# Performance work log

Hardware: AMD Instinct MI355X
Metric: run time of the kernel (lower is better)

## Reference

```python
import jax, jax.numpy as jnp
import numpy as np
import math

B, S, H, N = 64, 512, 768, 16
C_COMP, C_REL = 5, 3
P = N * (N - 1)
LN_EPS = 1e-5

# ordered pair indices (i, j), i != j, row-major like the torch double loop
_PAIR_I, _PAIR_J = np.nonzero(~np.eye(N, dtype=bool))
_PAIR_I = jnp.asarray(_PAIR_I)
_PAIR_J = jnp.asarray(_PAIR_J)


def setup_inputs() -> dict:
    key = jax.random.key(0)
    ks = jax.random.split(key, 20)
    sc = 0.02
    p = lambda k, shape: (jax.random.normal(k, shape, jnp.float32) * sc)
    return {
        "last_hidden_state": jax.random.normal(ks[0], (B, S, H), jnp.float32),
        "span_starts": jax.random.randint(ks[1], (B, N), 0, 480).astype(jnp.int32),
        "span_lengths": jax.random.randint(ks[2], (B, N), 0, 31).astype(jnp.int32),
        "components": jax.random.randint(ks[3], (B, N), 0, C_COMP).astype(jnp.int32),
        "relations": jax.random.randint(ks[4], (B, P), 0, C_REL).astype(jnp.int32),
        # comp_classifier: Linear(H,512) -> Tanh -> Linear(512,C_COMP)
        "comp_w1": p(ks[5], (H, 512)), "comp_b1": jnp.zeros((512,), jnp.float32),
        "comp_w2": p(ks[6], (512, C_COMP)), "comp_b2": jnp.zeros((C_COMP,), jnp.float32),
        # Attention(H, H), no bias
        "wq": p(ks[7], (H, H)), "wk": p(ks[8], (H, H)), "wv": p(ks[9], (H, H)),
        # LayerNorm(H)
        "ln_g": jnp.ones((H,), jnp.float32), "ln_b": jnp.zeros((H,), jnp.float32),
        # rel_classifier: Linear(2H,512) -> Tanh -> Linear(512,C_REL)
        "rel_w1": p(ks[10], (2 * H, 512)), "rel_b1": jnp.zeros((512,), jnp.float32),
        "rel_w2": p(ks[11], (512, C_REL)), "rel_b2": jnp.zeros((C_REL,), jnp.float32),
    }


def _ce_mean(logits, gold):
    # logits [M, C], gold [M] -> scalar mean cross entropy
    logp = jax.nn.log_softmax(logits, axis=-1)
    return -jnp.mean(jnp.take_along_axis(logp, gold[:, None].astype(jnp.int32), axis=-1))


def reference(last_hidden_state, span_starts, span_lengths, components, relations,
              comp_w1, comp_b1, comp_w2, comp_b2,
              wq, wk, wv, ln_g, ln_b,
              rel_w1, rel_b1, rel_w2, rel_b2):
    # --- per-span mean pooling (inclusive end = start + length), masked+vectorized ---
    pos = jnp.arange(S)
    ends = span_starts + span_lengths
    mask = ((pos[None, None, :] >= span_starts[:, :, None]) &
            (pos[None, None, :] <= ends[:, :, None])).astype(jnp.float32)  # [B,N,S]
    lens = (span_lengths + 1).astype(jnp.float32)
    pooled = jnp.einsum('bns,bsh->bnh', mask, last_hidden_state) / lens[:, :, None]  # [B,N,H]
    # dropout(p=0.2) is identity in eval mode

    # --- component classifier ---
    comp_logits = jnp.tanh(pooled @ comp_w1 + comp_b1) @ comp_w2 + comp_b2  # [B,N,C_COMP]

    # --- small self-attention over spans ---
    q = pooled @ wq; k = pooled @ wk; v = pooled @ wv
    scores = jax.nn.softmax(jnp.einsum('bnd,bmd->bnm', q, k) / math.sqrt(H), axis=-1)
    attn = jnp.einsum('bnm,bmh->bnh', scores, v)

    # --- residual + layernorm ---
    x = pooled + attn
    mu = jnp.mean(x, axis=-1, keepdims=True)
    var = jnp.mean((x - mu) ** 2, axis=-1, keepdims=True)
    x = (x - mu) * jax.lax.rsqrt(var + LN_EPS) * ln_g + ln_b  # [B,N,H]

    # --- O(N^2) pairwise relation classification (ordered pairs i != j) ---
    pair_feat = jnp.concatenate([x[:, _PAIR_I, :], x[:, _PAIR_J, :]], axis=-1)  # [B,P,2H]
    rel_logits = jnp.tanh(pair_feat @ rel_w1 + rel_b1) @ rel_w2 + rel_b2  # [B,P,C_REL]

    loss_comp = _ce_mean(comp_logits.reshape(-1, C_COMP), components.reshape(-1))
    loss_rel = _ce_mean(rel_logits.reshape(-1, C_REL), relations.reshape(-1))
    return (comp_logits.reshape(-1, C_COMP), rel_logits.reshape(-1, C_REL), loss_comp, loss_rel)
```

## Files before the change

### kernel.cpp

```cpp
#include <hip/hip_runtime.h>

#define BB 64
#define SS 512
#define HH 768
#define PP 240
#define CCOMP 5

typedef unsigned short u16;
typedef __attribute__((ext_vector_type(8))) short bf16x8;
typedef __attribute__((ext_vector_type(4))) float f32x4;

__device__ __forceinline__ u16 f2bf(float f) {
    union { float f; unsigned int i; } v; v.f = f;
    unsigned int x = v.i;
    unsigned int lsb = (x >> 16) & 1u;
    x += 0x7fffu + lsb;
    return (u16)(x >> 16);
}

__device__ __forceinline__ float ftanh(float x) {
    float xc = fminf(fmaxf(x, -15.f), 15.f);
    float e = __expf(2.f * xc);
    return (e - 1.f) / (e + 1.f);
}

__device__ __forceinline__ void gl_lds16(const void* g, void* l) {
    __builtin_amdgcn_global_load_lds(
        (const __attribute__((address_space(1))) unsigned int*)g,
        (__attribute__((address_space(3))) unsigned int*)l, 16, 0, 0);
}

__global__ __launch_bounds__(256) void prep_pool_kernel(
    const float* __restrict__ lhs, const int* __restrict__ starts,
    const int* __restrict__ lens, float* __restrict__ pooled, u16* __restrict__ pooled_bf,
    const float* __restrict__ cw1, const float* __restrict__ wq,
    const float* __restrict__ wk, const float* __restrict__ wv,
    const float* __restrict__ rw1, u16* __restrict__ wcat_t, u16* __restrict__ relw_t) {
    int blk = blockIdx.x;
    int tid = threadIdx.x;
    if (blk < 1024) {
        if (tid >= 192) return;
        int st = starts[blk];
        int ln = lens[blk];
        int b = blk >> 4;
        const float4* base = (const float4*)(lhs + ((size_t)b * SS + st) * HH);
        float4 a = {0.f, 0.f, 0.f, 0.f};
        for (int s = 0; s <= ln; ++s) {
            float4 v = base[s * 192 + tid];
            a.x += v.x; a.y += v.y; a.z += v.z; a.w += v.w;
        }
        float inv = 1.0f / (float)(ln + 1);
        a.x *= inv; a.y *= inv; a.z *= inv; a.w *= inv;
        *(float4*)(pooled + (size_t)blk * HH + tid * 4) = a;
        ushort4 ub = { f2bf(a.x), f2bf(a.y), f2bf(a.z), f2bf(a.w) };
        *(ushort4*)(pooled_bf + (size_t)blk * HH + tid * 4) = ub;
        return;
    }
    blk -= 1024;
    const float* W; int ldw, nt; u16* outp;
    if (blk < 384)        {             W = cw1; ldw = 512; nt = 16; outp = wcat_t; }
    else if (blk < 960)   { blk -= 384; W = wq;  ldw = 768; nt = 24; outp = wcat_t + (size_t)512 * 768; }
    else if (blk < 1536)  { blk -= 960; W = wk;  ldw = 768; nt = 24; outp = wcat_t + (size_t)1280 * 768; }
    else if (blk < 2112)  { blk -= 1536; W = wv; ldw = 768; nt = 24; outp = wcat_t + (size_t)2048 * 768; }
    else if (blk < 2496)  { blk -= 2112; W = rw1; ldw = 512; nt = 16; outp = relw_t; }
    else                  { blk -= 2496; W = rw1 + (size_t)768 * 512; ldw = 512; nt = 16; outp = relw_t + (size_t)512 * 768; }
    int tk = blk / nt, tn = blk % nt;
    int k0 = tk * 32, n0 = tn * 32;
    __shared__ u16 Ls[32][36];
    int tx = tid & 31, ty = tid >> 5;
#pragma unroll
    for (int r = 0; r < 4; ++r) {
        int k = ty + r * 8;
        Ls[tx][k] = f2bf(W[(size_t)(k0 + k) * ldw + n0 + tx]);
    }
    __syncthreads();
#pragma unroll
    for (int r = 0; r < 4; ++r) {
        int n = ty + r * 8;
        outp[(size_t)(n0 + n) * 768 + k0 + tx] = Ls[n][tx];
    }
}

__global__ __launch_bounds__(256) void gemm_pw_kernel(
    const u16* __restrict__ pooled_bf, const u16* __restrict__ wcat_t,
    const float* __restrict__ comp_b1, float* __restrict__ y2) {
    __shared__ u16 As[2][4096];
    __shared__ u16 Bs[2][4096];
    int bid = blockIdx.x;
    int sw = (bid & 7) * 88 + (bid >> 3);
    int ct = sw >> 4;
    int rt = sw & 15;
    int ccol0 = ct * 64, row0 = rt * 64;
    int act = (ccol0 < 512);
    int tid = threadIdx.x;
    int lane = tid & 63, w = tid >> 6;
    int q = lane >> 4, l15 = lane & 15;
    int wm = (w & 1) * 32, wn = (w >> 1) * 32;

    int srow = w * 8 + (lane >> 3);
    int sxs = ((lane & 7) * 16) ^ ((srow & 7) << 4);
    const char* gA0 = (const char*)(pooled_bf + (size_t)(row0 + srow) * 768) + sxs;
    const char* gA1 = gA0 + (size_t)32 * 768 * 2;
    const char* gB0 = (const char*)(wcat_t + (size_t)(ccol0 + srow) * 768) + sxs;
    const char* gB1 = gB0 + (size_t)32 * 768 * 2;
    char* lA = (char*)As + w * 1024;
    char* lB = (char*)Bs + w * 1024;

    f32x4 acc[2][2];
#pragma unroll
    for (int i = 0; i < 2; ++i)
#pragma unroll
        for (int j = 0; j < 2; ++j) acc[i][j] = (f32x4){0.f, 0.f, 0.f, 0.f};

#define STAGE_PW(BUF, KB) do { \
        gl_lds16(gA0 + (KB), lA + (BUF) * 8192); \
        gl_lds16(gA1 + (KB), lA + (BUF) * 8192 + 4096); \
        gl_lds16(gB0 + (KB), lB + (BUF) * 8192); \
        gl_lds16(gB1 + (KB), lB + (BUF) * 8192 + 4096); \
    } while (0)

    STAGE_PW(0, 0);
    asm volatile("s_waitcnt vmcnt(0)" ::: "memory");
    __syncthreads();
    int cur = 0;
    for (int t = 0; t < 12; ++t) {
        if (t < 11) STAGE_PW(cur ^ 1, (t + 1) * 128);
        const char* Ab = (const char*)As + cur * 8192;
        const char* Bb = (const char*)Bs + cur * 8192;
#pragma unroll
        for (int ks = 0; ks < 2; ++ks) {
            int o = ks * 64 + q * 16;
            int Ra0 = wm + l15, Ra1 = wm + 16 + l15;
            int Rb0 = wn + l15, Rb1 = wn + 16 + l15;
            bf16x8 a0 = *(const bf16x8*)(Ab + Ra0 * 128 + (o ^ ((Ra0 & 7) << 4)));
            bf16x8 a1 = *(const bf16x8*)(Ab + Ra1 * 128 + (o ^ ((Ra1 & 7) << 4)));
            bf16x8 b0 = *(const bf16x8*)(Bb + Rb0 * 128 + (o ^ ((Rb0 & 7) << 4)));
            bf16x8 b1 = *(const bf16x8*)(Bb + Rb1 * 128 + (o ^ ((Rb1 & 7) << 4)));
            acc[0][0] = __builtin_amdgcn_mfma_f32_16x16x32_bf16(a0, b0, acc[0][0], 0, 0, 0);
            acc[0][1] = __builtin_amdgcn_mfma_f32_16x16x32_bf16(a0, b1, acc[0][1], 0, 0, 0);
            acc[1][0] = __builtin_amdgcn_mfma_f32_16x16x32_bf16(a1, b0, acc[1][0], 0, 0, 0);
            acc[1][1] = __builtin_amdgcn_mfma_f32_16x16x32_bf16(a1, b1, acc[1][1], 0, 0, 0);
        }
        asm volatile("s_waitcnt vmcnt(0)" ::: "memory");
        __syncthreads();
        cur ^= 1;
    }
#pragma unroll
    for (int tm = 0; tm < 2; ++tm)
#pragma unroll
        for (int tn = 0; tn < 2; ++tn)
#pragma unroll
            for (int reg = 0; reg < 4; ++reg) {
                int rr = row0 + wm + tm * 16 + q * 4 + reg;
                int cc = ccol0 + wn + tn * 16 + l15;
                float v = acc[tm][tn][reg];
                if (act) v = ftanh(v + comp_b1[cc]);
                y2[(size_t)rr * 2816 + cc] = v;
            }
}

__global__ __launch_bounds__(256) void gemm_z_kernel(
    const u16* __restrict__ x_bf, const u16* __restrict__ relw_t, float* __restrict__ Z) {
    __shared__ u16 As[2][4096];
    __shared__ u16 Bs[2][4096];
    int bid = blockIdx.x;
    int sw = (bid & 7) * 32 + (bid >> 3);
    int ct = sw >> 4;
    int rt = sw & 15;
    int ccol0 = ct * 64, row0 = rt * 64;
    int tid = threadIdx.x;
    int lane = tid & 63, w = tid >> 6;
    int q = lane >> 4, l15 = lane & 15;
    int wm = (w & 1) * 32, wn = (w >> 1) * 32;

    int srow = w * 8 + (lane >> 3);
    int sxs = ((lane & 7) * 16) ^ ((srow & 7) << 4);
    const char* gA0 = (const char*)(x_bf + (size_t)(row0 + srow) * 768) + sxs;
    const char* gA1 = gA0 + (size_t)32 * 768 * 2;
    const char* gB0 = (const char*)(relw_t + (size_t)(ccol0 + srow) * 768) + sxs;
    const char* gB1 = gB0 + (size_t)32 * 768 * 2;
    char* lA = (char*)As + w * 1024;
    char* lB = (char*)Bs + w * 1024;

    f32x4 acc[2][2];
#pragma unroll
    for (int i = 0; i < 2; ++i)
#pragma unroll
        for (int j = 0; j < 2; ++j) acc[i][j] = (f32x4){0.f, 0.f, 0.f, 0.f};

    STAGE_PW(0, 0);
    asm volatile("s_waitcnt vmcnt(0)" ::: "memory");
    __syncthreads();
    int cur = 0;
    for (int t = 0; t < 12; ++t) {
        if (t < 11) STAGE_PW(cur ^ 1, (t + 1) * 128);
        const char* Ab = (const char*)As + cur * 8192;
        const char* Bb = (const char*)Bs + cur * 8192;
#pragma unroll
        for (int ks = 0; ks < 2; ++ks) {
            int o = ks * 64 + q * 16;
            int Ra0 = wm + l15, Ra1 = wm + 16 + l15;
            int Rb0 = wn + l15, Rb1 = wn + 16 + l15;
            bf16x8 a0 = *(const bf16x8*)(Ab + Ra0 * 128 + (o ^ ((Ra0 & 7) << 4)));
            bf16x8 a1 = *(const bf16x8*)(Ab + Ra1 * 128 + (o ^ ((Ra1 & 7) << 4)));
            bf16x8 b0 = *(const bf16x8*)(Bb + Rb0 * 128 + (o ^ ((Rb0 & 7) << 4)));
            bf16x8 b1 = *(const bf16x8*)(Bb + Rb1 * 128 + (o ^ ((Rb1 & 7) << 4)));
            acc[0][0] = __builtin_amdgcn_mfma_f32_16x16x32_bf16(a0, b0, acc[0][0], 0, 0, 0);
            acc[0][1] = __builtin_amdgcn_mfma_f32_16x16x32_bf16(a0, b1, acc[0][1], 0, 0, 0);
            acc[1][0] = __builtin_amdgcn_mfma_f32_16x16x32_bf16(a1, b0, acc[1][0], 0, 0, 0);
            acc[1][1] = __builtin_amdgcn_mfma_f32_16x16x32_bf16(a1, b1, acc[1][1], 0, 0, 0);
        }
        asm volatile("s_waitcnt vmcnt(0)" ::: "memory");
        __syncthreads();
        cur ^= 1;
    }
#pragma unroll
    for (int tm = 0; tm < 2; ++tm)
#pragma unroll
        for (int tn = 0; tn < 2; ++tn)
#pragma unroll
            for (int reg = 0; reg < 4; ++reg) {
                int rr = row0 + wm + tm * 16 + q * 4 + reg;
                int cc = ccol0 + wn + tn * 16 + l15;
                Z[(size_t)rr * 1024 + cc] = acc[tm][tn][reg];
            }
}

__global__ __launch_bounds__(256) void attn_ln_kernel(
    const float* __restrict__ y2, const float* __restrict__ pooled,
    const float* __restrict__ ln_g, const float* __restrict__ ln_b,
    u16* __restrict__ x_bf) {
    int w = threadIdx.x >> 6, l = threadIdx.x & 63;
    int gw = blockIdx.x * 4 + w;
    int b = gw >> 4, n = gw & 15;
    const float* qrow = y2 + (size_t)(b * 16 + n) * 2816 + 512;
    float qv[12];
#pragma unroll
    for (int u = 0; u < 12; ++u) qv[u] = qrow[l + 64 * u];

    float s[16];
#pragma unroll
    for (int m = 0; m < 16; ++m) {
        const float* krow = y2 + (size_t)(b * 16 + m) * 2816 + 1280;
        float p = 0.f;
#pragma unroll
        for (int u = 0; u < 12; ++u) p += qv[u] * krow[l + 64 * u];
#pragma unroll
        for (int off = 32; off >= 1; off >>= 1) p += __shfl_xor(p, off);
        s[m] = p * 0.03608439182435161f;
    }
    float mx = s[0];
#pragma unroll
    for (int m = 1; m < 16; ++m) mx = fmaxf(mx, s[m]);
    float den = 0.f;
#pragma unroll
    for (int m = 0; m < 16; ++m) { s[m] = __expf(s[m] - mx); den += s[m]; }
    float inv = 1.0f / den;

    float acc[12];
#pragma unroll
    for (int u = 0; u < 12; ++u) acc[u] = 0.f;
#pragma unroll
    for (int m = 0; m < 16; ++m) {
        const float* vrow = y2 + (size_t)(b * 16 + m) * 2816 + 2048;
        float pm = s[m] * inv;
#pragma unroll
        for (int u = 0; u < 12; ++u) acc[u] += pm * vrow[l + 64 * u];
    }

    int row = b * 16 + n;
    const float* prow = pooled + (size_t)row * HH;
    float xv[12];
    float ssum = 0.f, ssq = 0.f;
#pragma unroll
    for (int u = 0; u < 12; ++u) {
        float v = prow[l + 64 * u] + acc[u];
        xv[u] = v;
        ssum += v;
        ssq += v * v;
    }
#pragma unroll
    for (int off = 32; off >= 1; off >>= 1) {
        ssum += __shfl_xor(ssum, off);
        ssq += __shfl_xor(ssq, off);
    }
    float mu = ssum * (1.0f / 768.0f);
    float var = ssq * (1.0f / 768.0f) - mu * mu;
    float rs = rsqrtf(var + 1e-5f);
    u16* xrow_bf = x_bf + (size_t)row * HH;
#pragma unroll
    for (int u = 0; u < 12; ++u) {
        int h = l + 64 * u;
        xrow_bf[h] = f2bf((xv[u] - mu) * rs * ln_g[h] + ln_b[h]);
    }
}

__global__ __launch_bounds__(256) void heads_kernel(
    const float* __restrict__ Z, const float* __restrict__ rb1,
    const float* __restrict__ rw2, const float* __restrict__ rb2,
    const int* __restrict__ rels,
    const float* __restrict__ y2, const float* __restrict__ cw2,
    const float* __restrict__ cb2, const int* __restrict__ comps,
    float* __restrict__ out, float* __restrict__ rel_p, float* __restrict__ comp_p) {
    __shared__ float red[4];
    int wave = threadIdx.x >> 6, lane = threadIdx.x & 63;
    if (blockIdx.x < 3840) {
        int row = blockIdx.x * 4 + wave;
        int b = row / PP;
        int p = row - b * PP;
        int i = p / 15;
        int jj = p - i * 15;
        int j = jj + (jj >= i ? 1 : 0);
        const float* z1 = Z + ((size_t)(b * 16 + i)) * 1024;
        const float* z2 = Z + ((size_t)(b * 16 + j)) * 1024 + 512;
        float a0 = 0.f, a1 = 0.f, a2 = 0.f;
#pragma unroll
        for (int t = 0; t < 2; ++t) {
            int c = (lane + (t << 6)) << 2;
            float4 zv1 = *(const float4*)(z1 + c);
            float4 zv2 = *(const float4*)(z2 + c);
            float4 bv  = *(const float4*)(rb1 + c);
            float4 w0 = *(const float4*)(rw2 + c * 3);
            float4 w1 = *(const float4*)(rw2 + c * 3 + 4);
            float4 w2 = *(const float4*)(rw2 + c * 3 + 8);
            float fw[12] = {w0.x, w0.y, w0.z, w0.w, w1.x, w1.y, w1.z, w1.w, w2.x, w2.y, w2.z, w2.w};
            float h0 = ftanh(zv1.x + zv2.x + bv.x);
            float h1 = ftanh(zv1.y + zv2.y + bv.y);
            float h2 = ftanh(zv1.z + zv2.z + bv.z);
            float h3 = ftanh(zv1.w + zv2.w + bv.w);
            a0 += h0 * fw[0] + h1 * fw[3] + h2 * fw[6] + h3 * fw[9];
            a1 += h0 * fw[1] + h1 * fw[4] + h2 * fw[7] + h3 * fw[10];
            a2 += h0 * fw[2] + h1 * fw[5] + h2 * fw[8] + h3 * fw[11];
        }
#pragma unroll
        for (int off = 32; off >= 1; off >>= 1) {
            a0 += __shfl_down(a0, off);
            a1 += __shfl_down(a1, off);
            a2 += __shfl_down(a2, off);
        }
        if (lane == 0) {
            float l0 = a0 + rb2[0];
            float l1 = a1 + rb2[1];
            float l2 = a2 + rb2[2];
            float mxv = fmaxf(l0, fmaxf(l1, l2));
            float se = __expf(l0 - mxv) + __expf(l1 - mxv) + __expf(l2 - mxv);
            float lse = __logf(se) + mxv;
            int g = rels[row];
            float lg = (g == 0) ? l0 : ((g == 1) ? l1 : l2);
            red[wave] = lse - lg;
            float* o = out + 5120 + (size_t)row * 3;
            o[0] = l0; o[1] = l1; o[2] = l2;
        }
        __syncthreads();
        if (threadIdx.x == 0) rel_p[blockIdx.x] = red[0] + red[1] + red[2] + red[3];
    } else {
        int row = (blockIdx.x - 3840) * 4 + wave;
        const float* hrow = y2 + (size_t)row * 2816;
        float acc[CCOMP] = {0.f, 0.f, 0.f, 0.f, 0.f};
#pragma unroll
        for (int t = 0; t < 2; ++t) {
            int c = (lane + (t << 6)) << 2;
            float4 hv = *(const float4*)(hrow + c);
            float4 g0 = *(const float4*)(cw2 + c * 5);
            float4 g1 = *(const float4*)(cw2 + c * 5 + 4);
            float4 g2 = *(const float4*)(cw2 + c * 5 + 8);
            float4 g3 = *(const float4*)(cw2 + c * 5 + 12);
            float4 g4 = *(const float4*)(cw2 + c * 5 + 16);
            float fw[20] = {g0.x, g0.y, g0.z, g0.w, g1.x, g1.y, g1.z, g1.w,
                            g2.x, g2.y, g2.z, g2.w, g3.x, g3.y, g3.z, g3.w,
                            g4.x, g4.y, g4.z, g4.w};
            float hh[4] = {hv.x, hv.y, hv.z, hv.w};
#pragma unroll
            for (int jj = 0; jj < 4; ++jj)
#pragma unroll
                for (int cc = 0; cc < CCOMP; ++cc) acc[cc] += hh[jj] * fw[5 * jj + cc];
        }
#pragma unroll
        for (int cc = 0; cc < CCOMP; ++cc)
#pragma unroll
            for (int off = 32; off >= 1; off >>= 1) acc[cc] += __shfl_down(acc[cc], off);
        if (lane == 0) {
            float lg[CCOMP];
            float mxv = -1e30f;
#pragma unroll
            for (int cc = 0; cc < CCOMP; ++cc) { lg[cc] = acc[cc] + cb2[cc]; mxv = fmaxf(mxv, lg[cc]); }
            float se = 0.f;
#pragma unroll
            for (int cc = 0; cc < CCOMP; ++cc) se += __expf(lg[cc] - mxv);
            float lse = __logf(se) + mxv;
            red[wave] = lse - lg[comps[row]];
#pragma unroll
            for (int cc = 0; cc < CCOMP; ++cc) out[row * CCOMP + cc] = lg[cc];
        }
        __syncthreads();
        if (threadIdx.x == 0) comp_p[blockIdx.x - 3840] = red[0] + red[1] + red[2] + red[3];
    }
}

__global__ __launch_bounds__(256) void finalize_kernel(
    const float* __restrict__ comp_p, const float* __restrict__ rel_p,
    float* __restrict__ out) {
    __shared__ float rc[4], rr[4];
    int tid = threadIdx.x;
    int wave = tid >> 6, lane = tid & 63;
    float sc = comp_p[tid];
    float sr = 0.f;
#pragma unroll
    for (int k = 0; k < 15; ++k) sr += rel_p[tid + k * 256];
#pragma unroll
    for (int off = 32; off >= 1; off >>= 1) {
        sc += __shfl_down(sc, off);
        sr += __shfl_down(sr, off);
    }
    if (lane == 0) { rc[wave] = sc; rr[wave] = sr; }
    __syncthreads();
    if (tid == 0) {
        out[51200] = (rc[0] + rc[1] + rc[2] + rc[3]) * (1.0f / 1024.0f);
        out[51201] = (rr[0] + rr[1] + rr[2] + rr[3]) * (1.0f / 15360.0f);
    }
}

extern "C" void kernel_launch(void* const* d_in, const int* in_sizes, int n_in,
                              void* d_out, int out_size, void* d_ws, size_t ws_size,
                              hipStream_t stream) {
    const float* lhs     = (const float*)d_in[0];
    const int* starts    = (const int*)d_in[1];
    const int* lens      = (const int*)d_in[2];
    const int* comps     = (const int*)d_in[3];
    const int* rels      = (const int*)d_in[4];
    const float* comp_w1 = (const float*)d_in[5];
    const float* comp_b1 = (const float*)d_in[6];
    const float* comp_w2 = (const float*)d_in[7];
    const float* comp_b2 = (const float*)d_in[8];
    const float* wq      = (const float*)d_in[9];
    const float* wk      = (const float*)d_in[10];
    const float* wv      = (const float*)d_in[11];
    const float* ln_g    = (const float*)d_in[12];
    const float* ln_b    = (const float*)d_in[13];
    const float* rel_w1  = (const float*)d_in[14];
    const float* rel_b1  = (const float*)d_in[15];
    const float* rel_w2  = (const float*)d_in[16];
    const float* rel_b2  = (const float*)d_in[17];
    float* out = (float*)d_out;
    float* ws = (float*)d_ws;

    float* pooled = ws;
    float* y2     = pooled + 786432;
    float* Z      = y2 + 2883584;
    float* comp_p = Z + 1048576;
    float* rel_p  = comp_p + 256;
    u16* pooled_bf = (u16*)(rel_p + 3840);
    u16* x_bf      = pooled_bf + 786432;
    u16* wcat_t    = x_bf + 786432;
    u16* relw_t    = wcat_t + 2162688;

    prep_pool_kernel<<<3904, 256, 0, stream>>>(lhs, starts, lens, pooled, pooled_bf,
                                               comp_w1, wq, wk, wv, rel_w1, wcat_t, relw_t);
    gemm_pw_kernel<<<704, 256, 0, stream>>>(pooled_bf, wcat_t, comp_b1, y2);
    attn_ln_kernel<<<256, 256, 0, stream>>>(y2, pooled, ln_g, ln_b, x_bf);
    gemm_z_kernel<<<256, 256, 0, stream>>>(x_bf, relw_t, Z);
    heads_kernel<<<4096, 256, 0, stream>>>(Z, rel_b1, rel_w2, rel_b2, rels,
                                           y2, comp_w2, comp_b2, comps,
                                           out, rel_p, comp_p);
    finalize_kernel<<<1, 256, 0, stream>>>(comp_p, rel_p, out);
}
```

Before: 232.7 us.

## Fuse component head into attention kernel and finalize into heads via last-block reduction

Moves the component-classifier second layer and its cross-entropy into the attention/LayerNorm kernel, writing per-row loss partials. The final loss reduction is folded into the relation heads kernel using an atomic counter, so the last block sums the partials, and the separate finalize launch is removed. The shared GEMM main loop is factored into a device helper. This saves one kernel launch and the component-head blocks, but adds a memset, an atomic fence, and extra work per wave in the attention kernel.

After: 324.2 us. +39.3%, slower.

```diff
diff --git a/kernel.cpp b/kernel.cpp
--- a/kernel.cpp
+++ b/kernel.cpp
@@ -1,6 +1,5 @@
 #include <hip/hip_runtime.h>
 
-#define BB 64
 #define SS 512
 #define HH 768
 #define PP 240
@@ -81,52 +80,42 @@
     }
 }
 
-__global__ __launch_bounds__(256) void gemm_pw_kernel(
-    const u16* __restrict__ pooled_bf, const u16* __restrict__ wcat_t,
-    const float* __restrict__ comp_b1, float* __restrict__ y2) {
-    __shared__ u16 As[2][4096];
-    __shared__ u16 Bs[2][4096];
-    int bid = blockIdx.x;
-    int sw = (bid & 7) * 88 + (bid >> 3);
-    int ct = sw >> 4;
-    int rt = sw & 15;
-    int ccol0 = ct * 64, row0 = rt * 64;
-    int act = (ccol0 < 512);
-    int tid = threadIdx.x;
+__device__ __forceinline__ void gemm_tile(
+    const u16* Abase, const u16* Bbase, u16* AsR, u16* BsR,
+    int row0, int ccol0, int tid, f32x4 acc[2][2]) {
     int lane = tid & 63, w = tid >> 6;
     int q = lane >> 4, l15 = lane & 15;
     int wm = (w & 1) * 32, wn = (w >> 1) * 32;
 
     int srow = w * 8 + (lane >> 3);
     int sxs = ((lane & 7) * 16) ^ ((srow & 7) << 4);
-    const char* gA0 = (const char*)(pooled_bf + (size_t)(row0 + srow) * 768) + sxs;
+    const char* gA0 = (const char*)(Abase + (size_t)(row0 + srow) * 768) + sxs;
     const char* gA1 = gA0 + (size_t)32 * 768 * 2;
-    const char* gB0 = (const char*)(wcat_t + (size_t)(ccol0 + srow) * 768) + sxs;
+    const char* gB0 = (const char*)(Bbase + (size_t)(ccol0 + srow) * 768) + sxs;
     const char* gB1 = gB0 + (size_t)32 * 768 * 2;
-    char* lA = (char*)As + w * 1024;
-    char* lB = (char*)Bs + w * 1024;
-
-    f32x4 acc[2][2];
+    char* lA = (char*)AsR + w * 1024;
+    char* lB = (char*)BsR + w * 1024;
+
 #pragma unroll
     for (int i = 0; i < 2; ++i)
 #pragma unroll
         for (int j = 0; j < 2; ++j) acc[i][j] = (f32x4){0.f, 0.f, 0.f, 0.f};
 
-#define STAGE_PW(BUF, KB) do { \
+#define STAGE_T(BUF, KB) do { \
         gl_lds16(gA0 + (KB), lA + (BUF) * 8192); \
         gl_lds16(gA1 + (KB), lA + (BUF) * 8192 + 4096); \
         gl_lds16(gB0 + (KB), lB + (BUF) * 8192); \
         gl_lds16(gB1 + (KB), lB + (BUF) * 8192 + 4096); \
     } while (0)
 
-    STAGE_PW(0, 0);
+    STAGE_T(0, 0);
     asm volatile("s_waitcnt vmcnt(0)" ::: "memory");
     __syncthreads();
     int cur = 0;
     for (int t = 0; t < 12; ++t) {
-        if (t < 11) STAGE_PW(cur ^ 1, (t + 1) * 128);
-        const char* Ab = (const char*)As + cur * 8192;
-        const char* Bb = (const char*)Bs + cur * 8192;
+        if (t < 11) STAGE_T(cur ^ 1, (t + 1) * 128);
+        const char* Ab = (const char*)AsR + cur * 8192;
+        const char* Bb = (const char*)BsR + cur * 8192;
 #pragma unroll
         for (int ks = 0; ks < 2; ++ks) {
             int o = ks * 64 + q * 16;
@@ -145,6 +134,25 @@
         __syncthreads();
         cur ^= 1;
     }
+#undef STAGE_T
+}
+
+__global__ __launch_bounds__(256) void gemm_pw_kernel(
+    const u16* __restrict__ pooled_bf, const u16* __restrict__ wcat_t,
+    const float* __restrict__ comp_b1, float* __restrict__ y2) {
+    __shared__ u16 As[2][4096];
+    __shared__ u16 Bs[2][4096];
+    int bid = blockIdx.x;
+    int sw = (bid & 7) * 88 + (bid >> 3);
+    int ct = sw >> 4, rt = sw & 15;
+    int ccol0 = ct * 64, row0 = rt * 64;
+    int act = (ccol0 < 512);
+    int tid = threadIdx.x;
+    int lane = tid & 63, w = tid >> 6;
+    int q = lane >> 4, l15 = lane & 15;
+    int wm = (w & 1) * 32, wn = (w >> 1) * 32;
+    f32x4 acc[2][2];
+    gemm_tile(pooled_bf, wcat_t, &As[0][0], &Bs[0][0], row0, ccol0, tid, acc);
 #pragma unroll
     for (int tm = 0; tm < 2; ++tm)
 #pragma unroll
@@ -159,61 +167,129 @@
             }
 }
 
+__global__ __launch_bounds__(256) void attn_ln_kernel(
+    const float* __restrict__ y2, const float* __restrict__ pooled,
+    const float* __restrict__ ln_g, const float* __restrict__ ln_b,
+    const float* __restrict__ cw2, const float* __restrict__ cb2,
+    const int* __restrict__ comps,
+    u16* __restrict__ x_bf, float* __restrict__ out, float* __restrict__ comp_p) {
+    int w = threadIdx.x >> 6, l = threadIdx.x & 63;
+    int gw = blockIdx.x * 4 + w;
+    int b = gw >> 4, n = gw & 15;
+    const float* qrow = y2 + (size_t)(b * 16 + n) * 2816 + 512;
+    float qv[12];
+#pragma unroll
+    for (int u = 0; u < 12; ++u) qv[u] = qrow[l + 64 * u];
+
+    float s[16];
+#pragma unroll
+    for (int m = 0; m < 16; ++m) {
+        const float* krow = y2 + (size_t)(b * 16 + m) * 2816 + 1280;
+        float pv = 0.f;
+#pragma unroll
+        for (int u = 0; u < 12; ++u) pv += qv[u] * krow[l + 64 * u];
+#pragma unroll
+        for (int off = 32; off >= 1; off >>= 1) pv += __shfl_xor(pv, off);
+        s[m] = pv * 0.03608439182435161f;
+    }
+    float mx = s[0];
+#pragma unroll
+    for (int m = 1; m < 16; ++m) mx = fmaxf(mx, s[m]);
+    float den = 0.f;
+#pragma unroll
+    for (int m = 0; m < 16; ++m) { s[m] = __expf(s[m] - mx); den += s[m]; }
+    float inv = 1.0f / den;
+
+    float acc[12];
+#pragma unroll
+    for (int u = 0; u < 12; ++u) acc[u] = 0.f;
+#pragma unroll
+    for (int m = 0; m < 16; ++m) {
+        const float* vrow = y2 + (size_t)(b * 16 + m) * 2816 + 2048;
+        float pm = s[m] * inv;
+#pragma unroll
+        for (int u = 0; u < 12; ++u) acc[u] += pm * vrow[l + 64 * u];
+    }
+
+    int row = b * 16 + n;
+    const float* prow = pooled + (size_t)row * HH;
+    float xv[12];
+    float ssum = 0.f, ssq = 0.f;
+#pragma unroll
+    for (int u = 0; u < 12; ++u) {
+        float v = prow[l + 64 * u] + acc[u];
+        xv[u] = v;
+        ssum += v;
+        ssq += v * v;
+    }
+#pragma unroll
+    for (int off = 32; off >= 1; off >>= 1) {
+        ssum += __shfl_xor(ssum, off);
+        ssq += __shfl_xor(ssq, off);
+    }
+    float mu = ssum * (1.0f / 768.0f);
+    float var = ssq * (1.0f / 768.0f) - mu * mu;
+    float rs = rsqrtf(var + 1e-5f);
+    u16* xrow_bf = x_bf + (size_t)row * HH;
+#pragma unroll
+    for (int u = 0; u < 12; ++u) {
+        int h = l + 64 * u;
+        xrow_bf[h] = f2bf((xv[u] - mu) * rs * ln_g[h] + ln_b[h]);
+    }
+
+    const float* hrow = y2 + (size_t)row * 2816;
+    float ac[CCOMP] = {0.f, 0.f, 0.f, 0.f, 0.f};
+#pragma unroll
+    for (int t = 0; t < 2; ++t) {
+        int c = (l + (t << 6)) << 2;
+        float4 hv = *(const float4*)(hrow + c);
+        float4 g0 = *(const float4*)(cw2 + c * 5);
+        float4 g1 = *(const float4*)(cw2 + c * 5 + 4);
+        float4 g2 = *(const float4*)(cw2 + c * 5 + 8);
+        float4 g3 = *(const float4*)(cw2 + c * 5 + 12);
+        float4 g4 = *(const float4*)(cw2 + c * 5 + 16);
+        float fw[20] = {g0.x, g0.y, g0.z, g0.w, g1.x, g1.y, g1.z, g1.w,
+                        g2.x, g2.y, g2.z, g2.w, g3.x, g3.y, g3.z, g3.w,
+                        g4.x, g4.y, g4.z, g4.w};
+        float hh[4] = {hv.x, hv.y, hv.z, hv.w};
+#pragma unroll
+        for (int jj = 0; jj < 4; ++jj)
+#pragma unroll
+            for (int cc = 0; cc < CCOMP; ++cc) ac[cc] += hh[jj] * fw[5 * jj + cc];
+    }
+#pragma unroll
+    for (int cc = 0; cc < CCOMP; ++cc)
+#pragma unroll
+        for (int off = 32; off >= 1; off >>= 1) ac[cc] += __shfl_down(ac[cc], off);
+    if (l == 0) {
+        float lg[CCOMP];
+        float mxv = -1e30f;
+#pragma unroll
+        for (int cc = 0; cc < CCOMP; ++cc) { lg[cc] = ac[cc] + cb2[cc]; mxv = fmaxf(mxv, lg[cc]); }
+        float se = 0.f;
+#pragma unroll
+        for (int cc = 0; cc < CCOMP; ++cc) se += __expf(lg[cc] - mxv);
+        float lse = __logf(se) + mxv;
+        comp_p[row] = lse - lg[comps[row]];
+#pragma unroll
+        for (int cc = 0; cc < CCOMP; ++cc) out[row * CCOMP + cc] = lg[cc];
+    }
+}
+
 __global__ __launch_bounds__(256) void gemm_z_kernel(
     const u16* __restrict__ x_bf, const u16* __restrict__ relw_t, float* __restrict__ Z) {
     __shared__ u16 As[2][4096];
     __shared__ u16 Bs[2][4096];
     int bid = blockIdx.x;
     int sw = (bid & 7) * 32 + (bid >> 3);
-    int ct = sw >> 4;
-    int rt = sw & 15;
+    int ct = sw >> 4, rt = sw & 15;
     int ccol0 = ct * 64, row0 = rt * 64;
     int tid = threadIdx.x;
     int lane = tid & 63, w = tid >> 6;
     int q = lane >> 4, l15 = lane & 15;
     int wm = (w & 1) * 32, wn = (w >> 1) * 32;
-
-    int srow = w * 8 + (lane >> 3);
-    int sxs = ((lane & 7) * 16) ^ ((srow & 7) << 4);
-    const char* gA0 = (const char*)(x_bf + (size_t)(row0 + srow) * 768) + sxs;
-    const char* gA1 = gA0 + (size_t)32 * 768 * 2;
-    const char* gB0 = (const char*)(relw_t + (size_t)(ccol0 + srow) * 768) + sxs;
-    const char* gB1 = gB0 + (size_t)32 * 768 * 2;
-    char* lA = (char*)As + w * 1024;
-    char* lB = (char*)Bs + w * 1024;
-
     f32x4 acc[2][2];
-#pragma unroll
-    for (int i = 0; i < 2; ++i)
-#pragma unroll
-        for (int j = 0; j < 2; ++j) acc[i][j] = (f32x4){0.f, 0.f, 0.f, 0.f};
-
-    STAGE_PW(0, 0);
-    asm volatile("s_waitcnt vmcnt(0)" ::: "memory");
-    __syncthreads();
-    int cur = 0;
-    for (int t = 0; t < 12; ++t) {
-        if (t < 11) STAGE_PW(cur ^ 1, (t + 1) * 128);
-        const char* Ab = (const char*)As + cur * 8192;
-        const char* Bb = (const char*)Bs + cur * 8192;
-#pragma unroll
-        for (int ks = 0; ks < 2; ++ks) {
-            int o = ks * 64 + q * 16;
-            int Ra0 = wm + l15, Ra1 = wm + 16 + l15;
-            int Rb0 = wn + l15, Rb1 = wn + 16 + l15;
-            bf16x8 a0 = *(const bf16x8*)(Ab + Ra0 * 128 + (o ^ ((Ra0 & 7) << 4)));
-            bf16x8 a1 = *(const bf16x8*)(Ab + Ra1 * 128 + (o ^ ((Ra1 & 7) << 4)));
-            bf16x8 b0 = *(const bf16x8*)(Bb + Rb0 * 128 + (o ^ ((Rb0 & 7) << 4)));
-            bf16x8 b1 = *(const bf16x8*)(Bb + Rb1 * 128 + (o ^ ((Rb1 & 7) << 4)));
-            acc[0][0] = __builtin_amdgcn_mfma_f32_16x16x32_bf16(a0, b0, acc[0][0], 0, 0, 0);
-            acc[0][1] = __builtin_amdgcn_mfma_f32_16x16x32_bf16(a0, b1, acc[0][1], 0, 0, 0);
-            acc[1][0] = __builtin_amdgcn_mfma_f32_16x16x32_bf16(a1, b0, acc[1][0], 0, 0, 0);
-            acc[1][1] = __builtin_amdgcn_mfma_f32_16x16x32_bf16(a1, b1, acc[1][1], 0, 0, 0);
-        }
-        asm volatile("s_waitcnt vmcnt(0)" ::: "memory");
-        __syncthreads();
-        cur ^= 1;
-    }
+    gemm_tile(x_bf, relw_t, &As[0][0], &Bs[0][0], row0, ccol0, tid, acc);
 #pragma unroll
     for (int tm = 0; tm < 2; ++tm)
 #pragma unroll
@@ -226,197 +302,85 @@
             }
 }
 
-__global__ __launch_bounds__(256) void attn_ln_kernel(
-    const float* __restrict__ y2, const float* __restrict__ pooled,
-    const float* __restrict__ ln_g, const float* __restrict__ ln_b,
-    u16* __restrict__ x_bf) {
-    int w = threadIdx.x >> 6, l = threadIdx.x & 63;
-    int gw = blockIdx.x * 4 + w;
-    int b = gw >> 4, n = gw & 15;
-    const float* qrow = y2 + (size_t)(b * 16 + n) * 2816 + 512;
-    float qv[12];
-#pragma unroll
-    for (int u = 0; u < 12; ++u) qv[u] = qrow[l + 64 * u];
-
-    float s[16];
-#pragma unroll
-    for (int m = 0; m < 16; ++m) {
-        const float* krow = y2 + (size_t)(b * 16 + m) * 2816 + 1280;
-        float p = 0.f;
-#pragma unroll
-        for (int u = 0; u < 12; ++u) p += qv[u] * krow[l + 64 * u];
-#pragma unroll
-        for (int off = 32; off >= 1; off >>= 1) p += __shfl_xor(p, off);
-        s[m] = p * 0.03608439182435161f;
-    }
-    float mx = s[0];
-#pragma unroll
-    for (int m = 1; m < 16; ++m) mx = fmaxf(mx, s[m]);
-    float den = 0.f;
-#pragma unroll
-    for (int m = 0; m < 16; ++m) { s[m] = __expf(s[m] - mx); den += s[m]; }
-    float inv = 1.0f / den;
-
-    float acc[12];
-#pragma unroll
-    for (int u = 0; u < 12; ++u) acc[u] = 0.f;
-#pragma unroll
-    for (int m = 0; m < 16; ++m) {
-        const float* vrow = y2 + (size_t)(b * 16 + m) * 2816 + 2048;
-        float pm = s[m] * inv;
-#pragma unroll
-        for (int u = 0; u < 12; ++u) acc[u] += pm * vrow[l + 64 * u];
-    }
-
-    int row = b * 16 + n;
-    const float* prow = pooled + (size_t)row * HH;
-    float xv[12];
-    float ssum = 0.f, ssq = 0.f;
-#pragma unroll
-    for (int u = 0; u < 12; ++u) {
-        float v = prow[l + 64 * u] + acc[u];
-        xv[u] = v;
-        ssum += v;
-        ssq += v * v;
-    }
-#pragma unroll
-    for (int off = 32; off >= 1; off >>= 1) {
-        ssum += __shfl_xor(ssum, off);
-        ssq += __shfl_xor(ssq, off);
-    }
-    float mu = ssum * (1.0f / 768.0f);
-    float var = ssq * (1.0f / 768.0f) - mu * mu;
-    float rs = rsqrtf(var + 1e-5f);
-    u16* xrow_bf = x_bf + (size_t)row * HH;
-#pragma unroll
-    for (int u = 0; u < 12; ++u) {
-        int h = l + 64 * u;
-        xrow_bf[h] = f2bf((xv[u] - mu) * rs * ln_g[h] + ln_b[h]);
-    }
-}
-
 __global__ __launch_bounds__(256) void heads_kernel(
     const float* __restrict__ Z, const float* __restrict__ rb1,
     const float* __restrict__ rw2, const float* __restrict__ rb2,
-    const int* __restrict__ rels,
-    const float* __restrict__ y2, const float* __restrict__ cw2,
-    const float* __restrict__ cb2, const int* __restrict__ comps,
-    float* __restrict__ out, float* __restrict__ rel_p, float* __restrict__ comp_p) {
-    __shared__ float red[4];
+    const int* __restrict__ rels, const float* __restrict__ comp_p,
+    float* __restrict__ out, float* __restrict__ rel_p, unsigned int* __restrict__ cnt) {
+    __shared__ float red[8];
+    __shared__ int isLast;
     int wave = threadIdx.x >> 6, lane = threadIdx.x & 63;
-    if (blockIdx.x < 3840) {
-        int row = blockIdx.x * 4 + wave;
-        int b = row / PP;
-        int p = row - b * PP;
-        int i = p / 15;
-        int jj = p - i * 15;
-        int j = jj + (jj >= i ? 1 : 0);
-        const float* z1 = Z + ((size_t)(b * 16 + i)) * 1024;
-        const float* z2 = Z + ((size_t)(b * 16 + j)) * 1024 + 512;
-        float a0 = 0.f, a1 = 0.f, a2 = 0.f;
-#pragma unroll
-        for (int t = 0; t < 2; ++t) {
-            int c = (lane + (t << 6)) << 2;
-            float4 zv1 = *(const float4*)(z1 + c);
-            float4 zv2 = *(const float4*)(z2 + c);
-            float4 bv  = *(const float4*)(rb1 + c);
-            float4 w0 = *(const float4*)(rw2 + c * 3);
-            float4 w1 = *(const float4*)(rw2 + c * 3 + 4);
-            float4 w2 = *(const float4*)(rw2 + c * 3 + 8);
-            float fw[12] = {w0.x, w0.y, w0.z, w0.w, w1.x, w1.y, w1.z, w1.w, w2.x, w2.y, w2.z, w2.w};
-            float h0 = ftanh(zv1.x + zv2.x + bv.x);
-            float h1 = ftanh(zv1.y + zv2.y + bv.y);
-            float h2 = ftanh(zv1.z + zv2.z + bv.z);
-            float h3 = ftanh(zv1.w + zv2.w + bv.w);
-            a0 += h0 * fw[0] + h1 * fw[3] + h2 * fw[6] + h3 * fw[9];
-            a1 += h0 * fw[1] + h1 * fw[4] + h2 * fw[7] + h3 * fw[10];
-            a2 += h0 * fw[2] + h1 * fw[5] + h2 * fw[8] + h3 * fw[11];
+    int row = blockIdx.x * 4 + wave;
+    int b = row / PP;
+    int p = row - b * PP;
+    int i = p / 15;
+    int jj = p - i * 15;
+    int j = jj + (jj >= i ? 1 : 0);
+    const float* z1 = Z + ((size_t)(b * 16 + i)) * 1024;
+    const float* z2 = Z + ((size_t)(b * 16 + j)) * 1024 + 512;
+    float a0 = 0.f, a1 = 0.f, a2 = 0.f;
+#pragma unroll
+    for (int t = 0; t < 2; ++t) {
+        int c = (lane + (t << 6)) << 2;
+        float4 zv1 = *(const float4*)(z1 + c);
+        float4 zv2 = *(const float4*)(z2 + c);
+        float4 bv  = *(const float4*)(rb1 + c);
+        float4 w0 = *(const float4*)(rw2 + c * 3);
+        float4 w1 = *(const float4*)(rw2 + c * 3 + 4);
+        float4 w2 = *(const float4*)(rw2 + c * 3 + 8);
+        float fw[12] = {w0.x, w0.y, w0.z, w0.w, w1.x, w1.y, w1.z, w1.w, w2.x, w2.y, w2.z, w2.w};
+        float h0 = ftanh(zv1.x + zv2.x + bv.x);
+        float h1 = ftanh(zv1.y + zv2.y + bv.y);
+        float h2 = ftanh(zv1.z + zv2.z + bv.z);
+        float h3 = ftanh(zv1.w + zv2.w + bv.w);
+        a0 += h0 * fw[0] + h1 * fw[3] + h2 * fw[6] + h3 * fw[9];
+        a1 += h0 * fw[1] + h1 * fw[4] + h2 * fw[7] + h3 * fw[10];
+        a2 += h0 * fw[2] + h1 * fw[5] + h2 * fw[8] + h3 * fw[11];
+    }
+#pragma unroll
+    for (int off = 32; off >= 1; off >>= 1) {
+        a0 += __shfl_down(a0, off);
+        a1 += __shfl_down(a1, off);
+        a2 += __shfl_down(a2, off);
+    }
+    if (lane == 0) {
+        float l0 = a0 + rb2[0];
+        float l1 = a1 + rb2[1];
+        float l2 = a2 + rb2[2];
+        float mxv = fmaxf(l0, fmaxf(l1, l2));
+        float se = __expf(l0 - mxv) + __expf(l1 - mxv) + __expf(l2 - mxv);
+        float lse = __logf(se) + mxv;
+        int g = rels[row];
+        float lg = (g == 0) ? l0 : ((g == 1) ? l1 : l2);
+        red[wave] = lse - lg;
+        float* o = out + 5120 + (size_t)row * 3;
+        o[0] = l0; o[1] = l1; o[2] = l2;
+    }
+    __syncthreads();
+    if (threadIdx.x == 0) {
+        rel_p[blockIdx.x] = red[0] + red[1] + red[2] + red[3];
+        unsigned int old = __hip_atomic_fetch_add(cnt, 1u, __ATOMIC_ACQ_REL, __HIP_MEMORY_SCOPE_AGENT);
+        isLast = (old == (unsigned int)(gridDim.x - 1));
+    }
+    __syncthreads();
+    if (isLast) {
+        __builtin_amdgcn_fence(__ATOMIC_ACQUIRE, "agent");
+        int tid = threadIdx.x;
+        float sc = comp_p[tid] + comp_p[tid + 256] + comp_p[tid + 512] + comp_p[tid + 768];
+        float sr = 0.f;
+#pragma unroll
+        for (int k = 0; k < 15; ++k) sr += rel_p[tid + k * 256];
+#pragma unroll
+        for (int off = 32; off >= 1; off >>= 1) {
+            sc += __shfl_down(sc, off);
+            sr += __shfl_down(sr, off);
         }
-#pragma unroll
-        for (int off = 32; off >= 1; off >>= 1) {
-            a0 += __shfl_down(a0, off);
-            a1 += __shfl_down(a1, off);
-            a2 += __shfl_down(a2, off);
+        if (lane == 0) { red[wave] = sc; red[4 + wave] = sr; }
+        __syncthreads();
+        if (tid == 0) {
+            out[51200] = (red[0] + red[1] + red[2] + red[3]) * (1.0f / 1024.0f);
+            out[51201] = (red[4] + red[5] + red[6] + red[7]) * (1.0f / 15360.0f);
         }
-        if (lane == 0) {
-            float l0 = a0 + rb2[0];
-            float l1 = a1 + rb2[1];
-            float l2 = a2 + rb2[2];
-            float mxv = fmaxf(l0, fmaxf(l1, l2));
-            float se = __expf(l0 - mxv) + __expf(l1 - mxv) + __expf(l2 - mxv);
-            float lse = __logf(se) + mxv;
-            int g = rels[row];
-            float lg = (g == 0) ? l0 : ((g == 1) ? l1 : l2);
-            red[wave] = lse - lg;
-            float* o = out + 5120 + (size_t)row * 3;
-            o[0] = l0; o[1] = l1; o[2] = l2;
-        }
-        __syncthreads();
-        if (threadIdx.x == 0) rel_p[blockIdx.x] = red[0] + red[1] + red[2] + red[3];
-    } else {
-        int row = (blockIdx.x - 3840) * 4 + wave;
-        const float* hrow = y2 + (size_t)row * 2816;
-        float acc[CCOMP] = {0.f, 0.f, 0.f, 0.f, 0.f};
-#pragma unroll
-        for (int t = 0; t < 2; ++t) {
-            int c = (lane + (t << 6)) << 2;
-            float4 hv = *(const float4*)(hrow + c);
-            float4 g0 = *(const float4*)(cw2 + c * 5);
-            float4 g1 = *(const float4*)(cw2 + c * 5 + 4);
-            float4 g2 = *(const float4*)(cw2 + c * 5 + 8);
-            float4 g3 = *(const float4*)(cw2 + c * 5 + 12);
-            float4 g4 = *(const float4*)(cw2 + c * 5 + 16);
-            float fw[20] = {g0.x, g0.y, g0.z, g0.w, g1.x, g1.y, g1.z, g1.w,
-                            g2.x, g2.y, g2.z, g2.w, g3.x, g3.y, g3.z, g3.w,
-                            g4.x, g4.y, g4.z, g4.w};
-            float hh[4] = {hv.x, hv.y, hv.z, hv.w};
-#pragma unroll
-            for (int jj = 0; jj < 4; ++jj)
-#pragma unroll
-                for (int cc = 0; cc < CCOMP; ++cc) acc[cc] += hh[jj] * fw[5 * jj + cc];
-        }
-#pragma unroll
-        for (int cc = 0; cc < CCOMP; ++cc)
-#pragma unroll
-            for (int off = 32; off >= 1; off >>= 1) acc[cc] += __shfl_down(acc[cc], off);
-        if (lane == 0) {
-            float lg[CCOMP];
-            float mxv = -1e30f;
-#pragma unroll
-            for (int cc = 0; cc < CCOMP; ++cc) { lg[cc] = acc[cc] + cb2[cc]; mxv = fmaxf(mxv, lg[cc]); }
-            float se = 0.f;
-#pragma unroll
-            for (int cc = 0; cc < CCOMP; ++cc) se += __expf(lg[cc] - mxv);
-            float lse = __logf(se) + mxv;
-            red[wave] = lse - lg[comps[row]];
-#pragma unroll
-            for (int cc = 0; cc < CCOMP; ++cc) out[row * CCOMP + cc] = lg[cc];
-        }
-        __syncthreads();
-        if (threadIdx.x == 0) comp_p[blockIdx.x - 3840] = red[0] + red[1] + red[2] + red[3];
-    }
-}
-
-__global__ __launch_bounds__(256) void finalize_kernel(
-    const float* __restrict__ comp_p, const float* __restrict__ rel_p,
-    float* __restrict__ out) {
-    __shared__ float rc[4], rr[4];
-    int tid = threadIdx.x;
-    int wave = tid >> 6, lane = tid & 63;
-    float sc = comp_p[tid];
-    float sr = 0.f;
-#pragma unroll
-    for (int k = 0; k < 15; ++k) sr += rel_p[tid + k * 256];
-#pragma unroll
-    for (int off = 32; off >= 1; off >>= 1) {
-        sc += __shfl_down(sc, off);
-        sr += __shfl_down(sr, off);
-    }
-    if (lane == 0) { rc[wave] = sc; rr[wave] = sr; }
-    __syncthreads();
-    if (tid == 0) {
-        out[51200] = (rc[0] + rc[1] + rc[2] + rc[3]) * (1.0f / 1024.0f);
-        out[51201] = (rr[0] + rr[1] + rr[2] + rr[3]) * (1.0f / 15360.0f);
     }
 }
 
@@ -448,19 +412,20 @@
     float* y2     = pooled + 786432;
     float* Z      = y2 + 2883584;
     float* comp_p = Z + 1048576;
-    float* rel_p  = comp_p + 256;
+    float* rel_p  = comp_p + 1024;
     u16* pooled_bf = (u16*)(rel_p + 3840);
     u16* x_bf      = pooled_bf + 786432;
     u16* wcat_t    = x_bf + 786432;
     u16* relw_t    = wcat_t + 2162688;
-
+    unsigned int* cnt = (unsigned int*)(ws + 8 * 1024 * 1024);
+
+    (void)hipMemsetAsync(cnt, 0, 64, stream);
     prep_pool_kernel<<<3904, 256, 0, stream>>>(lhs, starts, lens, pooled, pooled_bf,
                                                comp_w1, wq, wk, wv, rel_w1, wcat_t, relw_t);
     gemm_pw_kernel<<<704, 256, 0, stream>>>(pooled_bf, wcat_t, comp_b1, y2);
-    attn_ln_kernel<<<256, 256, 0, stream>>>(y2, pooled, ln_g, ln_b, x_bf);
+    attn_ln_kernel<<<256, 256, 0, stream>>>(y2, pooled, ln_g, ln_b,
+                                            comp_w2, comp_b2, comps, x_bf, out, comp_p);
     gemm_z_kernel<<<256, 256, 0, stream>>>(x_bf, relw_t, Z);
-    heads_kernel<<<4096, 256, 0, stream>>>(Z, rel_b1, rel_w2, rel_b2, rels,
-                                           y2, comp_w2, comp_b2, comps,
-                                           out, rel_p, comp_p);
-    finalize_kernel<<<1, 256, 0, stream>>>(comp_p, rel_p, out);
-}
+    heads_kernel<<<3840, 256, 0, stream>>>(Z, rel_b1, rel_w2, rel_b2, rels, comp_p,
+                                           out, rel_p, cnt);
+}
```
